# Kernel optimization log

Measured on AMD Instinct MI355X. Metric: run time of the kernel, lower is better.

## Reference

```python
import jax, jax.numpy as jnp
import numpy as np

L = 2          # loopnum
BS = 64        # batch
T = 512        # tracklength
EC = 1024      # ecnum
CA1 = 1024     # ca1num
CA3 = 1024     # ca3num
ACT = 2        # actnum
TS = 0.1
SIGMA = 5.0    # ca3sigma


def setup_inputs() -> dict:
    key = jax.random.key(0)
    ks = jax.random.split(key, 10)
    return {
        "cue_ec3input": jax.random.normal(ks[0], (BS, T, EC), dtype=jnp.float32),
        "ec3_last": jax.random.uniform(ks[1], (L, BS, EC), dtype=jnp.float32),
        "ec5_last": jax.random.uniform(ks[2], (L, BS, EC), dtype=jnp.float32),
        "ca1_last": jax.random.uniform(ks[3], (L, BS, CA1), dtype=jnp.float32),
        # per-loop parameters, stacked on leading loop axis (mirrors nn.ModuleList)
        "wca3ca1": jax.random.uniform(ks[4], (L, CA3, CA1), dtype=jnp.float32) * 0.01,
        "wec3ca1": jax.random.normal(ks[5], (L, EC, CA1), dtype=jnp.float32) * 0.03,   # ~xavier scale
        "wca1ec5": jax.random.normal(ks[6], (L, CA1, EC), dtype=jnp.float32) * 0.03,
        "ca1bias": jnp.zeros((L, CA1), dtype=jnp.float32),
        "ec5bias": jnp.zeros((L, EC), dtype=jnp.float32),
        # interLayer i: nn.Linear(ca1num, ecnum) -> weight (EC, CA1), bias (EC,)
        "inter_w": jax.random.normal(ks[7], (L, EC, CA1), dtype=jnp.float32) * 0.02,
        "inter_b": jnp.zeros((L, EC), dtype=jnp.float32),
        "wca1act": jax.random.normal(ks[8], (CA1, ACT), dtype=jnp.float32) * 0.03,
        "actbias": jnp.zeros((ACT,), dtype=jnp.float32),
    }


def reference(cue_ec3input, ec3_last, ec5_last, ca1_last,
              wca3ca1, wec3ca1, wca1ec5, ca1bias, ec5bias,
              inter_w, inter_b, wca1act, actbias):
    ca3center = jnp.linspace(0.0, float(T), CA3)          # (CA3,)
    positions = jnp.arange(T, dtype=jnp.float32)          # (T,)
    cue_t = jnp.swapaxes(cue_ec3input, 0, 1)              # (T, BS, EC)

    def step(carry, xin):
        ec3, ec5, ca1 = carry                             # each (L, BS, dim)
        x, cue_x = xin                                    # scalar, (BS, EC)
        ca3 = jnp.exp(-(ca3center - x) ** 2 / (2.0 * SIGMA ** 2))  # (CA3,)
        ec3input = cue_x
        new_ec3, new_ec5, new_ca1 = [], [], []
        for i in range(L):                                # fixed, structurally distinct loops
            ca1_i = jax.nn.relu(
                jax.nn.sigmoid(10.0 * (ca3 @ wca3ca1[i] - 0.5))           # (CA1,)
                * (1.0 + 3.0 * jax.nn.sigmoid(ec3[i] @ wec3ca1[i]))       # (BS, CA1)
                - ca1bias[i]
            )
            ec5_i = ec5[i] + 10.0 * TS * (ca1_i @ wca1ec5[i]) + ec5bias[i]
            ec5_i = 0.69 + 0.3 * jax.nn.sigmoid(4.0 * (ec5_i - 0.3))
            ec3_i = ec5_i * ec3[i] + 0.6 * ec3input
            ec3input = ca1_i @ inter_w[i].T + inter_b[i]  # feed next loop
            new_ec3.append(ec3_i); new_ec5.append(ec5_i); new_ca1.append(ca1_i)
        ec3 = jnp.stack(new_ec3); ec5 = jnp.stack(new_ec5); ca1 = jnp.stack(new_ca1)
        # histories record batch element 0 only, as in the original
        hist = (ec3[:, 0, :], ec5[:, 0, :], ca1[:, 0, :])
        return (ec3, ec5, ca1), hist

    (ec3, ec5, ca1), (ec3his, ec5his, ca1his) = jax.lax.scan(
        step, (ec3_last, ec5_last, ca1_last), (positions, cue_t))

    # scan stacks on axis 0 -> (T, L, dim); original layout is (L, T, dim)
    ec3his = jnp.swapaxes(ec3his, 0, 1)
    ec5his = jnp.swapaxes(ec5his, 0, 1)
    ca1his = jnp.swapaxes(ca1his, 0, 1)

    actCell = ca1[-1] @ wca1act + actbias                 # (BS, ACT)
    return actCell, ec3his, ec5his, ca1his
```

## Files before the change

kernel.cpp:

```cpp
#include <hip/hip_runtime.h>

#define Lnum 2
#define BSn  64
#define Tn   512
#define ECn  1024
#define CA1n 1024
#define CHUNK 16

typedef short bf16x8 __attribute__((ext_vector_type(8)));
typedef float f32x4  __attribute__((ext_vector_type(4)));

#define MFMA16(a,b,c) __builtin_amdgcn_mfma_f32_16x16x32_bf16((a),(b),(c),0,0,0)

#define OUT_E3  128
#define OUT_E5  (128 + Lnum*Tn*ECn)
#define OUT_CA1 (128 + 2*Lnum*Tn*ECn)

#define WS_FLAGS 0
#define WS_EC3S  8192
#define WS_CA1S  4202496
#define WS_EC5F  8396800
#define WS_EC3F  8921088
#define WS_CA1L  9445376
#define WS_S     9707520
#define WS_W1T   11804672
#define WS_W2T   15998976
#define WS_W3T   20193280

#define AST(p, v) __hip_atomic_store((p), (v), __ATOMIC_RELAXED, __HIP_MEMORY_SCOPE_AGENT)
#define AADD(p, v) __hip_atomic_fetch_add((p), (v), __ATOMIC_RELAXED, __HIP_MEMORY_SCOPE_AGENT)
#define ALD(p)    __hip_atomic_load((p), __ATOMIC_RELAXED, __HIP_MEMORY_SCOPE_AGENT)

__device__ __forceinline__ float sigm(float x) { return 1.0f / (1.0f + __expf(-x)); }

__device__ __forceinline__ unsigned f2bfu(float f) {
  unsigned u = __float_as_uint(f);
  u += 0x7fffu + ((u >> 16) & 1u);
  return u >> 16;
}
__device__ __forceinline__ short f2bf(float f) { return (short)f2bfu(f); }
__device__ __forceinline__ float bf2f(short s) {
  return __uint_as_float(((unsigned)(unsigned short)s) << 16);
}

__device__ __forceinline__ void pollCnt(const unsigned* c, unsigned need) {
  while (ALD(c) < need) __builtin_amdgcn_s_sleep(1);
  __builtin_amdgcn_sched_barrier(0);
  asm volatile("" ::: "memory");
}
__device__ __forceinline__ void pollCnt2(const unsigned* c0, const unsigned* c1,
                                         unsigned need) {
  while ((ALD(c0) < need) | (ALD(c1) < need)) __builtin_amdgcn_s_sleep(1);
  __builtin_amdgcn_sched_barrier(0);
  asm volatile("" ::: "memory");
}
__device__ __forceinline__ void publish(unsigned* c) {
  asm volatile("s_waitcnt vmcnt(0)" ::: "memory");
  __syncthreads();
  if (threadIdx.x == 0)
    __hip_atomic_fetch_add(c, 1u, __ATOMIC_RELAXED, __HIP_MEMORY_SCOPE_AGENT);
}


__global__ void prep_state(const float* __restrict__ ec3_last,
                           const float* __restrict__ ec5_last,
                           unsigned* __restrict__ flags, unsigned* __restrict__ ec3su,
                           float* __restrict__ ec5f, float* __restrict__ ec3f) {
  int i = blockIdx.x * blockDim.x + threadIdx.x;
  if (i < 2048) flags[i] = 0u;
  float v3 = ec3_last[i];
  ec3f[i] = v3;
  ec5f[i] = ec5_last[i];
  if (i < Lnum * BSn * 512) {
    float lo = ec3_last[2 * i], hi = ec3_last[2 * i + 1];
    AST(ec3su + 15 * 65536 + i, f2bfu(lo) | (f2bfu(hi) << 16));
  }
}

__global__ void prep_wt(const float* __restrict__ w1, const float* __restrict__ w2,
                        short* __restrict__ w1t, short* __restrict__ w2t) {
  __shared__ float tile[64][65];
  const int b = blockIdx.x;
  const int m  = b >> 9;
  const int li = (b >> 8) & 1;
  const int kt = (b >> 4) & 15;
  const int ct = b & 15;
  const float* src = (m == 0 ? w1 : w2) + li * (1024 * 1024);
  short* dst = (m == 0 ? w1t : w2t) + li * (1024 * 1024);
#pragma unroll
  for (int i = 0; i < 16; ++i) {
    int idx = threadIdx.x + i * 256;
    int r = idx >> 6, c = idx & 63;
    tile[r][c] = src[(kt * 64 + r) * 1024 + ct * 64 + c];
  }
  __syncthreads();
#pragma unroll
  for (int i = 0; i < 16; ++i) {
    int idx = threadIdx.x + i * 256;
    int c = idx >> 6, r = idx & 63;
    dst[(ct * 64 + c) * 1024 + kt * 64 + r] = f2bf(tile[r][c]);
  }
}

__global__ void prep_w3(const float* __restrict__ inter_w, short* __restrict__ w3t) {
  int i = blockIdx.x * blockDim.x + threadIdx.x;
  w3t[i] = f2bf(inter_w[i]);
}

__global__ void prep_ca3(const float* __restrict__ wca3ca1, short* __restrict__ S) {
  const int t = blockIdx.x >> 1, li = blockIdx.x & 1;
  __shared__ float gauss[192];
  const float stepc = 512.0f / 1023.0f;
  const float tf = (float)t;
  int kmin = (int)floorf((tf - 40.0f) / stepc) - 1; if (kmin < 0) kmin = 0;
  int kmax = (int)ceilf((tf + 40.0f) / stepc) + 1;  if (kmax > 1023) kmax = 1023;
  int nw = kmax - kmin + 1;
  for (int j = threadIdx.x; j < nw; j += 256) {
    float d = (float)(kmin + j) * stepc - tf;
    gauss[j] = __expf(-d * d * 0.02f);
  }
  __syncthreads();
  const float* W = wca3ca1 + li * (1024 * 1024);
  for (int c = threadIdx.x; c < 1024; c += 256) {
    float s = 0.0f;
    for (int j = 0; j < nw; ++j) s += gauss[j] * W[(kmin + j) * 1024 + c];
    S[(li * Tn + t) * 1024 + c] = f2bf(sigm(10.0f * (s - 0.5f)));
  }
}

__global__ void __launch_bounds__(256, 1) stepchunk(
    const float* __restrict__ cue,
    const short* __restrict__ w1t, const short* __restrict__ w2t,
    const short* __restrict__ w3t, const short* __restrict__ stab,
    const float* __restrict__ ca1bias, const float* __restrict__ ec5bias,
    const float* __restrict__ interb,
    unsigned* __restrict__ flags, short* __restrict__ ec3s,
    short* __restrict__ ca1s, float* __restrict__ ec5f, float* __restrict__ ec3f,
    float* __restrict__ ca1l, float* __restrict__ out, int t0) {
  extern __shared__ short lds[];
  short* BT1 = lds;
  short* BT2 = lds + 16 * 1024;
  short* BT3 = lds + 32 * 1024;
  float* hist = (float*)(lds + 48 * 1024);

  unsigned* cntA0 = flags;
  unsigned* cntA1 = flags + 16;
  unsigned* cntB0 = flags + 32;
  unsigned* cntB1 = flags + 48;
  unsigned* ec3su = (unsigned*)ec3s;
  unsigned* ca1su = (unsigned*)ca1s;

  const int b = blockIdx.x;
  const int li = b & 1;
  const int c0 = (b >> 1) << 4;
  const int tid = threadIdx.x;
  const int lane = tid & 63, wave = tid >> 6;
  const int fr = lane & 15, ks = lane >> 4;
  const int r0 = wave << 4;
  const int ccol = c0 + fr;

  unsigned* myCntA = li ? cntA1 : cntA0;
  unsigned* myCntB = li ? cntB1 : cntB0;

  {
    int cp = tid & 15;
    int k0 = (tid >> 4) << 6;
    int xm = (cp & 7) << 3;
    const short* s1 = w1t + li * 1048576 + (c0 + cp) * 1024;
    const short* s2 = w2t + li * 1048576 + (c0 + cp) * 1024;
#pragma unroll
    for (int j = 0; j < 8; ++j) {
      int k = k0 + j * 8;
      *(bf16x8*)(BT1 + cp * 1024 + (k ^ xm)) = *(const bf16x8*)(s1 + k);
      *(bf16x8*)(BT2 + cp * 1024 + (k ^ xm)) = *(const bf16x8*)(s2 + k);
    }
    if (li == 1) {
      const short* s3 = w3t + (c0 + cp) * 1024;
#pragma unroll
      for (int j = 0; j < 8; ++j) {
        int k = k0 + j * 8;
        *(bf16x8*)(BT3 + cp * 1024 + (k ^ xm)) = *(const bf16x8*)(s3 + k);
      }
    }
  }
  __syncthreads();

  const int xsw = (fr & 7) << 3;
  const short* B1 = BT1 + fr * 1024;
  const short* B2 = BT2 + fr * 1024;
  const short* B3 = BT3 + fr * 1024;

  const float cb  = ca1bias[li * 1024 + ccol];
  const float e5b = ec5bias[li * 1024 + ccol];
  const float ib0 = interb[1024 + ccol];

  float e5r[4], e3r[4];
#pragma unroll
  for (int r = 0; r < 4; ++r) {
    int sidx = li * 65536 + (r0 + ks * 4 + r) * 1024 + ccol;
    e5r[r] = ec5f[sidx];
    e3r[r] = ec3f[sidx];
  }

  bf16x8 ar[32], ar3[32];
  f32x4 cvv;

  for (int tt = 0; tt < CHUNK; ++tt) {
    const int t = t0 + tt;
    const int rd = (tt + 15) & 15;

    const float g = bf2f(stab[(li * Tn + t) * 1024 + ccol]);
    float cueq[4];
    if (li == 0) {
#pragma unroll
      for (int r = 0; r < 4; ++r)
        cueq[r] = cue[((r0 + ks * 4 + r) * Tn + t) * 1024 + ccol];
    }

    {
      if (wave == 0) pollCnt(myCntB, 64u * (unsigned)t);
      __syncthreads();
      const short* A1 = ec3s + ((rd * 2 + li) * 64 + (r0 + fr)) * 1024 + ks * 8;
#pragma unroll
      for (int kk = 0; kk < 16; ++kk) {
        ar[kk]      = *(const bf16x8*)(A1 + kk * 32);
        ar[16 + kk] = *(const bf16x8*)(A1 + 512 + kk * 32);
      }
      __builtin_amdgcn_sched_barrier(0);
      f32x4 a0 = {0.f,0.f,0.f,0.f}, a1 = {0.f,0.f,0.f,0.f};
#pragma unroll
      for (int kk = 0; kk < 16; ++kk) {
        a0 = MFMA16(ar[kk],      *(const bf16x8*)(B1 + ((kk * 32 + ks * 8) ^ xsw)),       a0);
        a1 = MFMA16(ar[16 + kk], *(const bf16x8*)(B1 + ((512 + kk * 32 + ks * 8) ^ xsw)), a1);
      }
      f32x4 acc = a0 + a1;
#pragma unroll
      for (int r = 0; r < 4; ++r) {
        int grow = r0 + ks * 4 + r;
        float cv = fmaxf(g * (1.0f + 3.0f * sigm(acc[r])) - cb, 0.0f);
        cvv[r] = cv;
        unsigned my = f2bfu(cv);
        unsigned pr = (unsigned)__shfl_xor((int)my, 1);
        if ((fr & 1) == 0)
          AST(ca1su + ((tt * 2 + li) * 64 + grow) * 512 + ((c0 + fr) >> 1), my | (pr << 16));
      }
      if (wave == 0 && ks == 0) hist[tt * 16 + fr] = cvv[0];
      publish(myCntA);
      if (t == Tn - 1 && li == 1) {
#pragma unroll
        for (int r = 0; r < 4; ++r)
          ca1l[(r0 + ks * 4 + r) * 1024 + ccol] = cvv[r];
      }
    }

    {
      if (wave == 0) {
        if (li == 0) pollCnt(cntA0, 64u * (unsigned)(t + 1));
        else         pollCnt2(cntA0, cntA1, 64u * (unsigned)(t + 1));
      }
      __syncthreads();
      const short* A2 = ca1s + ((tt * 2 + li) * 64 + (r0 + fr)) * 1024 + ks * 8;
#pragma unroll
      for (int kk = 0; kk < 16; ++kk) {
        ar[kk]      = *(const bf16x8*)(A2 + kk * 32);
        ar[16 + kk] = *(const bf16x8*)(A2 + 512 + kk * 32);
      }
      if (li == 1) {
        const short* A3 = ca1s + ((tt * 2) * 64 + (r0 + fr)) * 1024 + ks * 8;
#pragma unroll
        for (int kk = 0; kk < 16; ++kk) {
          ar3[kk]      = *(const bf16x8*)(A3 + kk * 32);
          ar3[16 + kk] = *(const bf16x8*)(A3 + 512 + kk * 32);
        }
      }
      __builtin_amdgcn_sched_barrier(0);
      f32x4 p0 = {0.f,0.f,0.f,0.f}, p1 = {0.f,0.f,0.f,0.f};
#pragma unroll
      for (int kk = 0; kk < 16; ++kk) {
        p0 = MFMA16(ar[kk],      *(const bf16x8*)(B2 + ((kk * 32 + ks * 8) ^ xsw)),       p0);
        p1 = MFMA16(ar[16 + kk], *(const bf16x8*)(B2 + ((512 + kk * 32 + ks * 8) ^ xsw)), p1);
      }
      f32x4 g2 = p0 + p1;

      f32x4 xin;
      if (li == 1) {
        f32x4 q0 = {0.f,0.f,0.f,0.f}, q1 = {0.f,0.f,0.f,0.f};
#pragma unroll
        for (int kk = 0; kk < 16; ++kk) {
          q0 = MFMA16(ar3[kk],      *(const bf16x8*)(B3 + ((kk * 32 + ks * 8) ^ xsw)),       q0);
          q1 = MFMA16(ar3[16 + kk], *(const bf16x8*)(B3 + ((512 + kk * 32 + ks * 8) ^ xsw)), q1);
        }
        f32x4 q = q0 + q1;
#pragma unroll
        for (int r = 0; r < 4; ++r) xin[r] = q[r] + ib0;
      } else {
#pragma unroll
        for (int r = 0; r < 4; ++r) xin[r] = cueq[r];
      }

#pragma unroll
      for (int r = 0; r < 4; ++r) {
        float raw = e5r[r] + g2[r] + e5b;
        float e5 = 0.69f + 0.3f * sigm(4.0f * (raw - 0.3f));
        e5r[r] = e5;
        float e3 = e5 * e3r[r] + 0.6f * xin[r];
        e3r[r] = e3;
        int grow = r0 + ks * 4 + r;
        unsigned my = f2bfu(e3);
        unsigned pr = (unsigned)__shfl_xor((int)my, 1);
        if ((fr & 1) == 0)
          AST(ec3su + ((tt * 2 + li) * 64 + grow) * 512 + ((c0 + fr) >> 1), my | (pr << 16));
      }
      if (wave == 0 && ks == 0) {
        hist[256 + tt * 16 + fr] = e5r[0];
        hist[512 + tt * 16 + fr] = e3r[0];
      }
      publish(myCntB);
    }
  }

  if (wave == 0) {
    for (int s = ks; s < CHUNK; s += 4) {
      int t = t0 + s;
      out[OUT_CA1 + (li * Tn + t) * 1024 + ccol] = hist[s * 16 + fr];
      out[OUT_E5  + (li * Tn + t) * 1024 + ccol] = hist[256 + s * 16 + fr];
      out[OUT_E3  + (li * Tn + t) * 1024 + ccol] = hist[512 + s * 16 + fr];
    }
  }
#pragma unroll
  for (int r = 0; r < 4; ++r) {
    int sidx = li * 65536 + (r0 + ks * 4 + r) * 1024 + ccol;
    ec5f[sidx] = e5r[r];
    ec3f[sidx] = e3r[r];
  }
}

__global__ void act_cell(const float* __restrict__ ca1l, const float* __restrict__ wca1act,
                         const float* __restrict__ actbias, float* __restrict__ out) {
  int tid = threadIdx.x;
  if (tid < 128) {
    int b = tid >> 1, a = tid & 1;
    float s = 0.0f;
    for (int k = 0; k < 1024; ++k) s += ca1l[b * 1024 + k] * wca1act[k * 2 + a];
    out[b * 2 + a] = s + actbias[a];
  }
}

extern "C" void kernel_launch(void* const* d_in, const int* in_sizes, int n_in,
                              void* d_out, int out_size, void* d_ws, size_t ws_size,
                              hipStream_t stream) {
  (void)in_sizes; (void)n_in; (void)out_size; (void)ws_size;
  const float* cue      = (const float*)d_in[0];
  const float* ec3_last = (const float*)d_in[1];
  const float* ec5_last = (const float*)d_in[2];
  const float* wca3ca1  = (const float*)d_in[4];
  const float* wec3ca1  = (const float*)d_in[5];
  const float* wca1ec5  = (const float*)d_in[6];
  const float* ca1bias  = (const float*)d_in[7];
  const float* ec5bias  = (const float*)d_in[8];
  const float* inter_w  = (const float*)d_in[9];
  const float* inter_b  = (const float*)d_in[10];
  const float* wca1act  = (const float*)d_in[11];
  const float* actbias  = (const float*)d_in[12];
  float* out = (float*)d_out;

  char* ws = (char*)d_ws;
  unsigned* flags = (unsigned*)(ws + WS_FLAGS);
  short* ec3s = (short*)(ws + WS_EC3S);
  short* ca1s = (short*)(ws + WS_CA1S);
  float* ec5f = (float*)(ws + WS_EC5F);
  float* ec3f = (float*)(ws + WS_EC3F);
  float* ca1l = (float*)(ws + WS_CA1L);
  short* stab = (short*)(ws + WS_S);
  short* w1t  = (short*)(ws + WS_W1T);
  short* w2t  = (short*)(ws + WS_W2T);
  short* w3t  = (short*)(ws + WS_W3T);

  prep_state<<<dim3(512), dim3(256), 0, stream>>>(ec3_last, ec5_last, flags,
                                                  (unsigned*)ec3s, ec5f, ec3f);
  prep_wt<<<dim3(1024), dim3(256), 0, stream>>>(wec3ca1, wca1ec5, w1t, w2t);
  prep_w3<<<dim3(4096), dim3(256), 0, stream>>>(inter_w, w3t);
  prep_ca3<<<dim3(1024), dim3(256), 0, stream>>>(wca3ca1, stab);

  hipFuncSetAttribute((const void*)stepchunk,
                      hipFuncAttributeMaxDynamicSharedMemorySize, 101376);

  for (int c = 0; c < Tn / CHUNK; ++c) {
    stepchunk<<<dim3(128), dim3(256), 101376, stream>>>(
        cue, w1t, w2t, w3t, stab, ca1bias, ec5bias, inter_b,
        flags, ec3s, ca1s, ec5f, ec3f, ca1l, out, c * CHUNK);
  }

  act_cell<<<dim3(1), dim3(128), 0, stream>>>(ca1l, wca1act, actbias, out);
}
```

Baseline: 8.092 ms.

## Widen column tiles, spread blocks across XCDs, and decouple inter-loop dependency

Each persistent block now computes 32 output columns instead of 16, which halves the number of participating blocks to 64 and the per-step barrier counts. Blocks are indexed so only li<2 within each group of 8 is active, which appears intended to place each loop's blocks on particular XCDs. Loop-1 blocks now wait on a separate counter that loop-0 blocks bump after republishing ca1 with atomic stores, rather than polling loop 0's A counter directly. The inter_w matrix is read from global memory instead of LDS so that two weight tiles fit in LDS. The cost is fewer blocks doing the work, more MFMA work per block, and extra redundant stores of ca1.

Measured after the change: 12.33 ms. +52.4%, slower.

```diff
diff --git a/kernel.cpp b/kernel.cpp
--- a/kernel.cpp
+++ b/kernel.cpp
@@ -57,8 +57,7 @@
 __device__ __forceinline__ void publish(unsigned* c) {
   asm volatile("s_waitcnt vmcnt(0)" ::: "memory");
   __syncthreads();
-  if (threadIdx.x == 0)
-    __hip_atomic_fetch_add(c, 1u, __ATOMIC_RELAXED, __HIP_MEMORY_SCOPE_AGENT);
+  if (threadIdx.x == 0) AADD(c, 1u);
 }
 
 
@@ -138,87 +137,87 @@
     short* __restrict__ ca1s, float* __restrict__ ec5f, float* __restrict__ ec3f,
     float* __restrict__ ca1l, float* __restrict__ out, int t0) {
   extern __shared__ short lds[];
+  const int b = blockIdx.x;
+  const int li = b & 7;
+  if (li >= Lnum) return;
   short* BT1 = lds;
-  short* BT2 = lds + 16 * 1024;
-  short* BT3 = lds + 32 * 1024;
-  float* hist = (float*)(lds + 48 * 1024);
+  short* BT2 = lds + 32 * 1024;
+  float* hist = (float*)(lds + 64 * 1024);
 
   unsigned* cntA0 = flags;
   unsigned* cntA1 = flags + 16;
   unsigned* cntB0 = flags + 32;
   unsigned* cntB1 = flags + 48;
+  unsigned* cntM  = flags + 64;
   unsigned* ec3su = (unsigned*)ec3s;
   unsigned* ca1su = (unsigned*)ca1s;
 
-  const int b = blockIdx.x;
-  const int li = b & 1;
-  const int c0 = (b >> 1) << 4;
+  const int wid = b >> 3;
+  const int c0 = wid << 5;
   const int tid = threadIdx.x;
   const int lane = tid & 63, wave = tid >> 6;
   const int fr = lane & 15, ks = lane >> 4;
   const int r0 = wave << 4;
-  const int ccol = c0 + fr;
+  const int cc0 = c0 + fr, cc1 = c0 + 16 + fr;
 
   unsigned* myCntA = li ? cntA1 : cntA0;
   unsigned* myCntB = li ? cntB1 : cntB0;
 
   {
-    int cp = tid & 15;
-    int k0 = (tid >> 4) << 6;
+    int cp = tid & 31;
+    int k0 = (tid >> 5) << 7;
     int xm = (cp & 7) << 3;
     const short* s1 = w1t + li * 1048576 + (c0 + cp) * 1024;
     const short* s2 = w2t + li * 1048576 + (c0 + cp) * 1024;
 #pragma unroll
-    for (int j = 0; j < 8; ++j) {
+    for (int j = 0; j < 16; ++j) {
       int k = k0 + j * 8;
       *(bf16x8*)(BT1 + cp * 1024 + (k ^ xm)) = *(const bf16x8*)(s1 + k);
       *(bf16x8*)(BT2 + cp * 1024 + (k ^ xm)) = *(const bf16x8*)(s2 + k);
     }
-    if (li == 1) {
-      const short* s3 = w3t + (c0 + cp) * 1024;
-#pragma unroll
-      for (int j = 0; j < 8; ++j) {
-        int k = k0 + j * 8;
-        *(bf16x8*)(BT3 + cp * 1024 + (k ^ xm)) = *(const bf16x8*)(s3 + k);
-      }
-    }
   }
   __syncthreads();
 
   const int xsw = (fr & 7) << 3;
-  const short* B1 = BT1 + fr * 1024;
-  const short* B2 = BT2 + fr * 1024;
-  const short* B3 = BT3 + fr * 1024;
-
-  const float cb  = ca1bias[li * 1024 + ccol];
-  const float e5b = ec5bias[li * 1024 + ccol];
-  const float ib0 = interb[1024 + ccol];
-
-  float e5r[4], e3r[4];
+  const short* B1a = BT1 + fr * 1024;
+  const short* B1b = BT1 + (16 + fr) * 1024;
+  const short* B2a = BT2 + fr * 1024;
+  const short* B2b = BT2 + (16 + fr) * 1024;
+  const short* W3a = w3t + cc0 * 1024 + ks * 8;
+  const short* W3b = w3t + cc1 * 1024 + ks * 8;
+
+  const float cb0 = ca1bias[li * 1024 + cc0], cb1 = ca1bias[li * 1024 + cc1];
+  const float e5b0 = ec5bias[li * 1024 + cc0], e5b1 = ec5bias[li * 1024 + cc1];
+  const float ib0v = interb[1024 + cc0], ib1v = interb[1024 + cc1];
+
+  float e5r0[4], e3r0[4], e5r1[4], e3r1[4];
 #pragma unroll
   for (int r = 0; r < 4; ++r) {
-    int sidx = li * 65536 + (r0 + ks * 4 + r) * 1024 + ccol;
-    e5r[r] = ec5f[sidx];
-    e3r[r] = ec3f[sidx];
-  }
-
-  bf16x8 ar[32], ar3[32];
-  f32x4 cvv;
+    int base = li * 65536 + (r0 + ks * 4 + r) * 1024;
+    e5r0[r] = ec5f[base + cc0]; e3r0[r] = ec3f[base + cc0];
+    e5r1[r] = ec5f[base + cc1]; e3r1[r] = ec3f[base + cc1];
+  }
+
+  bf16x8 ar[32];
+  f32x4 cv0, cv1;
 
   for (int tt = 0; tt < CHUNK; ++tt) {
     const int t = t0 + tt;
     const int rd = (tt + 15) & 15;
 
-    const float g = bf2f(stab[(li * Tn + t) * 1024 + ccol]);
-    float cueq[4];
+    const float g0 = bf2f(stab[(li * Tn + t) * 1024 + cc0]);
+    const float g1 = bf2f(stab[(li * Tn + t) * 1024 + cc1]);
+    float cq0[4], cq1[4];
     if (li == 0) {
 #pragma unroll
-      for (int r = 0; r < 4; ++r)
-        cueq[r] = cue[((r0 + ks * 4 + r) * Tn + t) * 1024 + ccol];
+      for (int r = 0; r < 4; ++r) {
+        cq0[r] = cue[((r0 + ks * 4 + r) * Tn + t) * 1024 + cc0];
+        cq1[r] = cue[((r0 + ks * 4 + r) * Tn + t) * 1024 + cc1];
+      }
     }
 
     {
-      if (wave == 0) pollCnt(myCntB, 64u * (unsigned)t);
+      if (wave == 0) pollCnt(myCntB, 32u * (unsigned)t);
       __syncthreads();
       const short* A1 = ec3s + ((rd * 2 + li) * 64 + (r0 + fr)) * 1024 + ks * 8;
 #pragma unroll
@@ -228,35 +227,62 @@
       }
       __builtin_amdgcn_sched_barrier(0);
       f32x4 a0 = {0.f,0.f,0.f,0.f}, a1 = {0.f,0.f,0.f,0.f};
+      f32x4 y0 = {0.f,0.f,0.f,0.f}, y1 = {0.f,0.f,0.f,0.f};
 #pragma unroll
       for (int kk = 0; kk < 16; ++kk) {
-        a0 = MFMA16(ar[kk],      *(const bf16x8*)(B1 + ((kk * 32 + ks * 8) ^ xsw)),       a0);
-        a1 = MFMA16(ar[16 + kk], *(const bf16x8*)(B1 + ((512 + kk * 32 + ks * 8) ^ xsw)), a1);
-      }
-      f32x4 acc = a0 + a1;
+        a0 = MFMA16(ar[kk],      *(const bf16x8*)(B1a + ((kk * 32 + ks * 8) ^ xsw)),       a0);
+        a1 = MFMA16(ar[16 + kk], *(const bf16x8*)(B1a + ((512 + kk * 32 + ks * 8) ^ xsw)), a1);
+        y0 = MFMA16(ar[kk],      *(const bf16x8*)(B1b + ((kk * 32 + ks * 8) ^ xsw)),       y0);
+        y1 = MFMA16(ar[16 + kk], *(const bf16x8*)(B1b + ((512 + kk * 32 + ks * 8) ^ xsw)), y1);
+      }
+      f32x4 acc0 = a0 + a1, acc1 = y0 + y1;
 #pragma unroll
       for (int r = 0; r < 4; ++r) {
         int grow = r0 + ks * 4 + r;
-        float cv = fmaxf(g * (1.0f + 3.0f * sigm(acc[r])) - cb, 0.0f);
-        cvv[r] = cv;
-        unsigned my = f2bfu(cv);
-        unsigned pr = (unsigned)__shfl_xor((int)my, 1);
-        if ((fr & 1) == 0)
-          AST(ca1su + ((tt * 2 + li) * 64 + grow) * 512 + ((c0 + fr) >> 1), my | (pr << 16));
-      }
-      if (wave == 0 && ks == 0) hist[tt * 16 + fr] = cvv[0];
+        float v0 = fmaxf(g0 * (1.0f + 3.0f * sigm(acc0[r])) - cb0, 0.0f);
+        float v1 = fmaxf(g1 * (1.0f + 3.0f * sigm(acc1[r])) - cb1, 0.0f);
+        cv0[r] = v0; cv1[r] = v1;
+        unsigned m0 = f2bfu(v0), m1 = f2bfu(v1);
+        unsigned p0_ = (unsigned)__shfl_xor((int)m0, 1);
+        unsigned p1_ = (unsigned)__shfl_xor((int)m1, 1);
+        if ((fr & 1) == 0) {
+          int rb = ((tt * 2 + li) * 64 + grow) * 512;
+          ca1su[rb + (cc0 >> 1)] = m0 | (p0_ << 16);
+          ca1su[rb + (cc1 >> 1)] = m1 | (p1_ << 16);
+        }
+      }
+      if (wave == 0 && ks == 0) {
+        hist[tt * 32 + fr] = cv0[0];
+        hist[tt * 32 + 16 + fr] = cv1[0];
+      }
       publish(myCntA);
       if (t == Tn - 1 && li == 1) {
 #pragma unroll
-        for (int r = 0; r < 4; ++r)
-          ca1l[(r0 + ks * 4 + r) * 1024 + ccol] = cvv[r];
+        for (int r = 0; r < 4; ++r) {
+          ca1l[(r0 + ks * 4 + r) * 1024 + cc0] = cv0[r];
+          ca1l[(r0 + ks * 4 + r) * 1024 + cc1] = cv1[r];
+        }
       }
     }
 
     {
+      if (li == 0) {
+#pragma unroll
+        for (int r = 0; r < 4; ++r) {
+          int grow = r0 + ks * 4 + r;
+          unsigned m0 = f2bfu(cv0[r]), m1 = f2bfu(cv1[r]);
+          unsigned p0_ = (unsigned)__shfl_xor((int)m0, 1);
+          unsigned p1_ = (unsigned)__shfl_xor((int)m1, 1);
+          if ((fr & 1) == 0) {
+            int rb = ((tt * 2) * 64 + grow) * 512;
+            AST(ca1su + rb + (cc0 >> 1), m0 | (p0_ << 16));
+            AST(ca1su + rb + (cc1 >> 1), m1 | (p1_ << 16));
+          }
+        }
+      }
       if (wave == 0) {
-        if (li == 0) pollCnt(cntA0, 64u * (unsigned)(t + 1));
-        else         pollCnt2(cntA0, cntA1, 64u * (unsigned)(t + 1));
+        if (li == 0) pollCnt(cntA0, 32u * (unsigned)(t + 1));
+        else         pollCnt2(cntA1, cntM, 32u * (unsigned)(t + 1));
       }
       __syncthreads();
       const short* A2 = ca1s + ((tt * 2 + li) * 64 + (r0 + fr)) * 1024 + ks * 8;
@@ -265,73 +291,84 @@
         ar[kk]      = *(const bf16x8*)(A2 + kk * 32);
         ar[16 + kk] = *(const bf16x8*)(A2 + 512 + kk * 32);
       }
+      __builtin_amdgcn_sched_barrier(0);
+      f32x4 p0 = {0.f,0.f,0.f,0.f}, p1 = {0.f,0.f,0.f,0.f};
+      f32x4 q0 = {0.f,0.f,0.f,0.f}, q1 = {0.f,0.f,0.f,0.f};
+#pragma unroll
+      for (int kk = 0; kk < 16; ++kk) {
+        p0 = MFMA16(ar[kk],      *(const bf16x8*)(B2a + ((kk * 32 + ks * 8) ^ xsw)),       p0);
+        p1 = MFMA16(ar[16 + kk], *(const bf16x8*)(B2a + ((512 + kk * 32 + ks * 8) ^ xsw)), p1);
+        q0 = MFMA16(ar[kk],      *(const bf16x8*)(B2b + ((kk * 32 + ks * 8) ^ xsw)),       q0);
+        q1 = MFMA16(ar[16 + kk], *(const bf16x8*)(B2b + ((512 + kk * 32 + ks * 8) ^ xsw)), q1);
+      }
+      f32x4 g2a = p0 + p1, g2b = q0 + q1;
+
+      f32x4 x3a = {0.f,0.f,0.f,0.f}, x3b = {0.f,0.f,0.f,0.f};
       if (li == 1) {
         const short* A3 = ca1s + ((tt * 2) * 64 + (r0 + fr)) * 1024 + ks * 8;
 #pragma unroll
         for (int kk = 0; kk < 16; ++kk) {
-          ar3[kk]      = *(const bf16x8*)(A3 + kk * 32);
-          ar3[16 + kk] = *(const bf16x8*)(A3 + 512 + kk * 32);
-        }
-      }
-      __builtin_amdgcn_sched_barrier(0);
-      f32x4 p0 = {0.f,0.f,0.f,0.f}, p1 = {0.f,0.f,0.f,0.f};
-#pragma unroll
-      for (int kk = 0; kk < 16; ++kk) {
-        p0 = MFMA16(ar[kk],      *(const bf16x8*)(B2 + ((kk * 32 + ks * 8) ^ xsw)),       p0);
-        p1 = MFMA16(ar[16 + kk], *(const bf16x8*)(B2 + ((512 + kk * 32 + ks * 8) ^ xsw)), p1);
-      }
-      f32x4 g2 = p0 + p1;
-
-      f32x4 xin;
-      if (li == 1) {
-        f32x4 q0 = {0.f,0.f,0.f,0.f}, q1 = {0.f,0.f,0.f,0.f};
+          ar[kk]      = *(const bf16x8*)(A3 + kk * 32);
+          ar[16 + kk] = *(const bf16x8*)(A3 + 512 + kk * 32);
+        }
+        __builtin_amdgcn_sched_barrier(0);
+        f32x4 u0 = {0.f,0.f,0.f,0.f}, u1 = {0.f,0.f,0.f,0.f};
+        f32x4 v0 = {0.f,0.f,0.f,0.f}, v1 = {0.f,0.f,0.f,0.f};
 #pragma unroll
         for (int kk = 0; kk < 16; ++kk) {
-          q0 = MFMA16(ar3[kk],      *(const bf16x8*)(B3 + ((kk * 32 + ks * 8) ^ xsw)),       q0);
-          q1 = MFMA16(ar3[16 + kk], *(const bf16x8*)(B3 + ((512 + kk * 32 + ks * 8) ^ xsw)), q1);
-        }
-        f32x4 q = q0 + q1;
-#pragma unroll
-        for (int r = 0; r < 4; ++r) xin[r] = q[r] + ib0;
-      } else {
-#pragma unroll
-        for (int r = 0; r < 4; ++r) xin[r] = cueq[r];
+          u0 = MFMA16(ar[kk],      *(const bf16x8*)(W3a + kk * 32),       u0);
+          u1 = MFMA16(ar[16 + kk], *(const bf16x8*)(W3a + 512 + kk * 32), u1);
+          v0 = MFMA16(ar[kk],      *(const bf16x8*)(W3b + kk * 32),       v0);
+          v1 = MFMA16(ar[16 + kk], *(const bf16x8*)(W3b + 512 + kk * 32), v1);
+        }
+        x3a = u0 + u1; x3b = v0 + v1;
       }
 
 #pragma unroll
       for (int r = 0; r < 4; ++r) {
-        float raw = e5r[r] + g2[r] + e5b;
-        float e5 = 0.69f + 0.3f * sigm(4.0f * (raw - 0.3f));
-        e5r[r] = e5;
-        float e3 = e5 * e3r[r] + 0.6f * xin[r];
-        e3r[r] = e3;
         int grow = r0 + ks * 4 + r;
-        unsigned my = f2bfu(e3);
-        unsigned pr = (unsigned)__shfl_xor((int)my, 1);
-        if ((fr & 1) == 0)
-          AST(ec3su + ((tt * 2 + li) * 64 + grow) * 512 + ((c0 + fr) >> 1), my | (pr << 16));
+        float raw0 = e5r0[r] + g2a[r] + e5b0;
+        float e50 = 0.69f + 0.3f * sigm(4.0f * (raw0 - 0.3f));
+        e5r0[r] = e50;
+        float xin0 = (li == 1) ? (x3a[r] + ib0v) : cq0[r];
+        float e30 = e50 * e3r0[r] + 0.6f * xin0;
+        e3r0[r] = e30;
+        float raw1 = e5r1[r] + g2b[r] + e5b1;
+        float e51 = 0.69f + 0.3f * sigm(4.0f * (raw1 - 0.3f));
+        e5r1[r] = e51;
+        float xin1 = (li == 1) ? (x3b[r] + ib1v) : cq1[r];
+        float e31 = e51 * e3r1[r] + 0.6f * xin1;
+        e3r1[r] = e31;
+        unsigned m0 = f2bfu(e30), m1 = f2bfu(e31);
+        unsigned pp0 = (unsigned)__shfl_xor((int)m0, 1);
+        unsigned pp1 = (unsigned)__shfl_xor((int)m1, 1);
+        if ((fr & 1) == 0) {
+          int rb = ((tt * 2 + li) * 64 + grow) * 512;
+          ec3su[rb + (cc0 >> 1)] = m0 | (pp0 << 16);
+          ec3su[rb + (cc1 >> 1)] = m1 | (pp1 << 16);
+        }
       }
       if (wave == 0 && ks == 0) {
-        hist[256 + tt * 16 + fr] = e5r[0];
-        hist[512 + tt * 16 + fr] = e3r[0];
+        hist[512 + tt * 32 + fr] = e5r0[0];  hist[512 + tt * 32 + 16 + fr] = e5r1[0];
+        hist[1024 + tt * 32 + fr] = e3r0[0]; hist[1024 + tt * 32 + 16 + fr] = e3r1[0];
       }
       publish(myCntB);
+      if (tid == 0 && li == 0) AADD(cntM, 1u);
     }
   }
 
-  if (wave == 0) {
-    for (int s = ks; s < CHUNK; s += 4) {
-      int t = t0 + s;
-      out[OUT_CA1 + (li * Tn + t) * 1024 + ccol] = hist[s * 16 + fr];
-      out[OUT_E5  + (li * Tn + t) * 1024 + ccol] = hist[256 + s * 16 + fr];
-      out[OUT_E3  + (li * Tn + t) * 1024 + ccol] = hist[512 + s * 16 + fr];
-    }
+  for (int idx = tid; idx < 512; idx += 256) {
+    int s = idx >> 5, col = idx & 31;
+    int t = t0 + s;
+    out[OUT_CA1 + (li * Tn + t) * 1024 + c0 + col] = hist[s * 32 + col];
+    out[OUT_E5  + (li * Tn + t) * 1024 + c0 + col] = hist[512 + s * 32 + col];
+    out[OUT_E3  + (li * Tn + t) * 1024 + c0 + col] = hist[1024 + s * 32 + col];
   }
 #pragma unroll
   for (int r = 0; r < 4; ++r) {
-    int sidx = li * 65536 + (r0 + ks * 4 + r) * 1024 + ccol;
-    ec5f[sidx] = e5r[r];
-    ec3f[sidx] = e3r[r];
+    int base = li * 65536 + (r0 + ks * 4 + r) * 1024;
+    ec5f[base + cc0] = e5r0[r]; ec3f[base + cc0] = e3r0[r];
+    ec5f[base + cc1] = e5r1[r]; ec3f[base + cc1] = e3r1[r];
   }
 }
 
@@ -383,10 +420,10 @@
   prep_ca3<<<dim3(1024), dim3(256), 0, stream>>>(wca3ca1, stab);
 
   hipFuncSetAttribute((const void*)stepchunk,
-                      hipFuncAttributeMaxDynamicSharedMemorySize, 101376);
+                      hipFuncAttributeMaxDynamicSharedMemorySize, 137216);
 
   for (int c = 0; c < Tn / CHUNK; ++c) {
-    stepchunk<<<dim3(128), dim3(256), 101376, stream>>>(
+    stepchunk<<<dim3(256), dim3(256), 137216, stream>>>(
         cue, w1t, w2t, w3t, stab, ca1bias, ec5bias, inter_b,
         flags, ec3s, ca1s, ec5f, ec3f, ca1l, out, c * CHUNK);
   }
```
